# Kernel tuning notes

Measured on AMD Instinct MI355X. Metric: run time of the kernel, lower is better.

Reference implementation:

```python
import jax, jax.numpy as jnp
import numpy as np

DIM = 1024
NUM_HEADS = 16
HEAD_DIM = DIM // NUM_HEADS


def _rope_tables(seq_len, dim, dtype):
    # matches llama_rotary_embedding: inv_freq over even indices of head_dim
    inv_freq = 1.0 / (10000.0 ** (jnp.arange(0, dim, 2, dtype=jnp.float32) / dim))
    t = jnp.arange(seq_len, dtype=jnp.float32)
    freqs = jnp.outer(t, inv_freq)  # [S, dim/2]
    return jnp.cos(freqs).astype(dtype), jnp.sin(freqs).astype(dtype)


def _apply_rope(x, cos_emb, sin_emb):
    # x: [B, H, S, hd]; takes interleaved halves, concatenates rotated halves
    x1 = x[..., 0::2]
    x2 = x[..., 1::2]
    return jnp.concatenate((x1 * cos_emb - x2 * sin_emb,
                            x1 * sin_emb + x2 * cos_emb), axis=-1)


def setup_inputs() -> dict:
    key = jax.random.key(0)
    k_x, k_qkv, k_out, k_b = jax.random.split(key, 4)
    B, S, D = 2, 2048, DIM
    x = jax.random.normal(k_x, (B, S, D), dtype=jnp.float32)
    # torch nn.Linear weights are [out_features, in_features]
    w_qkv = jax.random.normal(k_qkv, (3 * D, D), dtype=jnp.float32) * (1.0 / np.sqrt(D))
    w_out = jax.random.normal(k_out, (D, D), dtype=jnp.float32) * (1.0 / np.sqrt(D))
    b_out = jax.random.normal(k_b, (D,), dtype=jnp.float32) * 0.01
    return {"x": x, "w_qkv": w_qkv, "w_out": w_out, "b_out": b_out}


def reference(x, w_qkv, w_out, b_out):
    B, S, D = x.shape
    H, hd = NUM_HEADS, HEAD_DIM
    qkv = jnp.einsum('bsd,ed->bse', x, w_qkv)  # [B, S, 3D]
    q, k, v = jnp.split(qkv, 3, axis=-1)
    # [B, S, D] -> [B, H, S, hd]
    q, k, v = (t.reshape(B, S, H, hd).transpose(0, 2, 1, 3) for t in (q, k, v))
    cos_emb, sin_emb = _rope_tables(S, hd, x.dtype)  # [S, hd/2]
    q = _apply_rope(q, cos_emb, sin_emb)
    k = _apply_rope(k, cos_emb, sin_emb)
    scores = jnp.einsum('bhqd,bhkd->bhqk', q, k) / jnp.sqrt(jnp.asarray(hd, x.dtype))
    attn = jax.nn.softmax(scores, axis=-1)
    out = jnp.einsum('bhqk,bhkd->bhqd', attn, v)
    out = out.transpose(0, 2, 1, 3).reshape(B, S, D)
    return jnp.einsum('bsd,ed->bse', out, w_out) + b_out
```

## Files before the change

### kernel.cpp

```cpp
#include <hip/hip_runtime.h>
#include <math.h>

typedef __bf16 bf16_t;
typedef bf16_t bf16x8 __attribute__((ext_vector_type(8)));
typedef bf16_t bf16x4 __attribute__((ext_vector_type(4)));
typedef short  s16x4  __attribute__((ext_vector_type(4)));
typedef float  f32x4  __attribute__((ext_vector_type(4)));

#define DIM_   1024
#define NHEADS 16
#define HDIM   64
#define SEQ    2048
#define BATCH  2

#define QK_SCALE 0.18033688011112042f

__device__ __forceinline__ s16x4 as_s16x4(bf16x4 v) {
    union { bf16x4 b; s16x4 s; } u; u.b = v; return u.s;
}

__device__ __forceinline__ void gld16(const bf16_t* g, bf16_t* l) {
    __builtin_amdgcn_global_load_lds(
        (const __attribute__((address_space(1))) void*)g,
        (__attribute__((address_space(3))) void*)l, 16, 0, 0);
}

#define XCNT   (4096u * 1024u)
#define WQCNT  (3072u * 1024u)
#define WOCNT  (1024u * 1024u)
__global__ __launch_bounds__(256) void cast3(const float* __restrict__ s0,
                                             const float* __restrict__ s1,
                                             const float* __restrict__ s2,
                                             bf16_t* __restrict__ d0,
                                             bf16_t* __restrict__ d1,
                                             bf16_t* __restrict__ d2) {
    size_t i = ((size_t)blockIdx.x * 256 + threadIdx.x) * 8;
    const float* s; bf16_t* d; size_t off;
    if (i < XCNT)               { s = s0; d = d0; off = i; }
    else if (i < XCNT + WQCNT)  { s = s1; d = d1; off = i - XCNT; }
    else                        { s = s2; d = d2; off = i - XCNT - WQCNT; }
    float4 a = *(const float4*)(s + off);
    float4 b = *(const float4*)(s + off + 4);
    bf16x8 o = { (bf16_t)a.x, (bf16_t)a.y, (bf16_t)a.z, (bf16_t)a.w,
                 (bf16_t)b.x, (bf16_t)b.y, (bf16_t)b.z, (bf16_t)b.w };
    *(bf16x8*)(d + off) = o;
}

template <bool QKV>
__global__ __launch_bounds__(256) void gemm_lds(const bf16_t* __restrict__ A,
                                                const bf16_t* __restrict__ B,
                                                const float* __restrict__ bias,
                                                void* __restrict__ Cout,
                                                bf16_t* __restrict__ vt,
                                                int M, int N, int K) {
    __shared__ __align__(16) bf16_t As[128 * 32];
    __shared__ __align__(16) bf16_t Bs[128 * 32];
    const int tid  = threadIdx.x;
    const int m0   = blockIdx.y * 128;
    const int n0   = blockIdx.x * 128;
    const int w    = tid >> 6;
    const int lane = tid & 63;
    const int m16  = lane & 15;
    const int quad = lane >> 4;
    const int wm   = (w >> 1) * 64;
    const int wn   = (w & 1) * 64;
    const int lrow = lane >> 2;
    const int lcol = (lane & 3) * 8;

    const bf16_t* pa0 = A + (size_t)(m0 + w * 16 + lrow) * K + lcol;
    const bf16_t* pb0 = B + (size_t)(n0 + w * 16 + lrow) * K + lcol;
    bf16_t* lA0 = &As[(w * 16) * 32];
    bf16_t* lA1 = &As[(64 + w * 16) * 32];
    bf16_t* lB0 = &Bs[(w * 16) * 32];
    bf16_t* lB1 = &Bs[(64 + w * 16) * 32];

    f32x4 acc[4][4] = {};

    for (int k0 = 0; k0 < K; k0 += 32) {
        __syncthreads();
        gld16(pa0 + k0, lA0);
        gld16(pa0 + (size_t)64 * K + k0, lA1);
        gld16(pb0 + k0, lB0);
        gld16(pb0 + (size_t)64 * K + k0, lB1);
        __syncthreads();

        bf16x8 af[4], bfr[4];
#pragma unroll
        for (int i = 0; i < 4; ++i)
            af[i] = *(const bf16x8*)(&As[(wm + i * 16 + m16) * 32 + quad * 8]);
#pragma unroll
        for (int j = 0; j < 4; ++j)
            bfr[j] = *(const bf16x8*)(&Bs[(wn + j * 16 + m16) * 32 + quad * 8]);
#pragma unroll
        for (int i = 0; i < 4; ++i)
#pragma unroll
            for (int j = 0; j < 4; ++j)
                acc[i][j] = __builtin_amdgcn_mfma_f32_16x16x32_bf16(af[i], bfr[j], acc[i][j], 0, 0, 0);
    }

    if (QKV && n0 >= 2 * DIM_) {
        const int b      = m0 >> 11;
        const int s_base = (m0 & (SEQ - 1)) + wm;
#pragma unroll
        for (int j = 0; j < 4; ++j) {
            const int cit = wn + j * 16 + m16;
            const int h   = ((n0 - 2 * DIM_) >> 6) + (cit >> 6);
            const int d   = cit & 63;
            bf16_t* vrow = vt + ((size_t)(b * 16 + h) * 64 + d) * SEQ + s_base;
#pragma unroll
            for (int i = 0; i < 4; ++i) {
                bf16x4 ov = { (bf16_t)acc[i][j][0], (bf16_t)acc[i][j][1],
                              (bf16_t)acc[i][j][2], (bf16_t)acc[i][j][3] };
                *(bf16x4*)(vrow + i * 16 + quad * 4) = ov;
            }
        }
    } else if (QKV) {
        bf16_t* C = (bf16_t*)Cout;
#pragma unroll
        for (int i = 0; i < 4; ++i)
#pragma unroll
            for (int j = 0; j < 4; ++j) {
                const int col = n0 + wn + j * 16 + m16;
#pragma unroll
                for (int r = 0; r < 4; ++r)
                    C[(size_t)(m0 + wm + i * 16 + quad * 4 + r) * N + col] = (bf16_t)acc[i][j][r];
            }
    } else {
        float* C = (float*)Cout;
#pragma unroll
        for (int j = 0; j < 4; ++j) {
            const int col = n0 + wn + j * 16 + m16;
            const float bv = bias[col];
#pragma unroll
            for (int i = 0; i < 4; ++i)
#pragma unroll
                for (int r = 0; r < 4; ++r)
                    C[(size_t)(m0 + wm + i * 16 + quad * 4 + r) * N + col] = acc[i][j][r] + bv;
        }
    }
}

__global__ __launch_bounds__(256) void rope_bf16(bf16_t* __restrict__ qkv) {
    __shared__ float ctab[8][32];
    __shared__ float stab[8][32];
    const int tid = threadIdx.x;
    const int sl  = tid >> 5, j = tid & 31;
    const int s   = (int)((blockIdx.x * 8 + sl) & (SEQ - 1));
    const float freq = exp2f(-0.41524101186092029f * (float)j);
    float sn, cs;
    sincosf((float)s * freq, &sn, &cs);
    ctab[sl][j] = cs;
    stab[sl][j] = sn;
    __syncthreads();

    const int gid   = blockIdx.x * 256 + tid;
    const int m     = gid >> 5;
    const int rr    = gid & 31;
    const int which = rr >> 4;
    const int hh    = rr & 15;
    const float osc = (which == 0) ? QK_SCALE : 1.0f;

    bf16_t* p = qkv + (size_t)m * (3 * DIM_) + which * DIM_ + hh * HDIM;
    union { bf16_t e[64]; bf16x8 v[8]; } X, O;
#pragma unroll
    for (int i = 0; i < 8; ++i) X.v[i] = *(const bf16x8*)(p + i * 8);
#pragma unroll
    for (int t = 0; t < 32; ++t) {
        const float x1 = (float)X.e[2 * t];
        const float x2 = (float)X.e[2 * t + 1];
        const float c  = ctab[sl][t];
        const float s2 = stab[sl][t];
        O.e[t]      = (bf16_t)((x1 * c - x2 * s2) * osc);
        O.e[32 + t] = (bf16_t)((x1 * s2 + x2 * c) * osc);
    }
#pragma unroll
    for (int i = 0; i < 8; ++i) *(bf16x8*)(p + i * 8) = O.v[i];
}

__global__ __launch_bounds__(256) void attn_mfma(const bf16_t* __restrict__ qkv,
                                                 const bf16_t* __restrict__ vt,
                                                 bf16_t* __restrict__ out) {
    __shared__ __align__(16) bf16_t Qs[64 * 72];
    __shared__ __align__(16) bf16_t Ks[64 * 72];
    __shared__ __align__(16) bf16_t Vt[64 * 72];

    const int tid  = threadIdx.x;
    const int w    = tid >> 6;
    const int lane = tid & 63;
    const int m16  = lane & 15;
    const int quad = lane >> 4;
    const int bh   = blockIdx.y;
    const int b    = bh >> 4;
    const int hh   = bh & 15;
    const int q0   = blockIdx.x * 64;

    const size_t rs = 3 * DIM_;
    const bf16_t* qbase = qkv + (size_t)(b * SEQ) * rs + hh * HDIM;
    const bf16_t* kbase = qbase + DIM_;
    const bf16_t* vtg   = vt + (size_t)bh * 64 * SEQ;

#pragma unroll
    for (int p = 0; p < 2; ++p) {
        const int idx = tid + p * 256;
        const int row = idx >> 3, c8 = (idx & 7) * 8;
        *(bf16x8*)(&Qs[row * 72 + c8]) =
            *(const bf16x8*)(qbase + (size_t)(q0 + row) * rs + c8);
    }
    __syncthreads();
    bf16x8 qf[2];
#pragma unroll
    for (int kt = 0; kt < 2; ++kt)
        qf[kt] = *(const bf16x8*)(&Qs[(w * 16 + m16) * 72 + kt * 32 + quad * 8]);

    f32x4 o[4] = {};
    float lp = 0.0f;

    for (int k0 = 0; k0 < SEQ; k0 += 64) {
#pragma unroll
        for (int p = 0; p < 2; ++p) {
            const int idx = tid + p * 256;
            const int row = idx >> 3, c8 = (idx & 7) * 8;
            *(bf16x8*)(&Ks[row * 72 + c8]) =
                *(const bf16x8*)(kbase + (size_t)(k0 + row) * rs + c8);
            *(bf16x8*)(&Vt[row * 72 + c8]) =
                *(const bf16x8*)(vtg + (size_t)row * SEQ + k0 + c8);
        }
        __syncthreads();

        f32x4 sc[4];
#pragma unroll
        for (int ks = 0; ks < 4; ++ks) {
            f32x4 c = {};
#pragma unroll
            for (int kt = 0; kt < 2; ++kt) {
                bf16x8 ak = *(const bf16x8*)(&Ks[(ks * 16 + m16) * 72 + kt * 32 + quad * 8]);
                c = __builtin_amdgcn_mfma_f32_16x16x32_bf16(ak, qf[kt], c, 0, 0, 0);
            }
            sc[ks] = c;
        }

        s16x4 pb[4];
#pragma unroll
        for (int ks = 0; ks < 4; ++ks) {
            bf16x4 pv;
#pragma unroll
            for (int r = 0; r < 4; ++r) {
                const float p = __builtin_amdgcn_exp2f(sc[ks][r]);
                lp += p;
                pv[r] = (bf16_t)p;
            }
            pb[ks] = as_s16x4(pv);
        }

#pragma unroll
        for (int ks = 0; ks < 4; ++ks) {
#pragma unroll
            for (int ds = 0; ds < 4; ++ds) {
                bf16x4 va = *(const bf16x4*)(&Vt[(ds * 16 + m16) * 72 + ks * 16 + quad * 4]);
                o[ds] = __builtin_amdgcn_mfma_f32_16x16x16bf16_1k(as_s16x4(va), pb[ks], o[ds], 0, 0, 0);
            }
        }
        __syncthreads();
    }

    lp += __shfl_xor(lp, 16);
    lp += __shfl_xor(lp, 32);
    const float inv = 1.0f / lp;

    const size_t token = (size_t)(b * SEQ + q0 + w * 16 + m16);
#pragma unroll
    for (int ds = 0; ds < 4; ++ds) {
        bf16x4 ov;
#pragma unroll
        for (int r = 0; r < 4; ++r) ov[r] = (bf16_t)(o[ds][r] * inv);
        *(bf16x4*)(out + token * DIM_ + hh * HDIM + ds * 16 + quad * 4) = ov;
    }
}

extern "C" void kernel_launch(void* const* d_in, const int* in_sizes, int n_in,
                              void* d_out, int out_size, void* d_ws, size_t ws_size,
                              hipStream_t stream) {
    const float* x     = (const float*)d_in[0];
    const float* w_qkv = (const float*)d_in[1];
    const float* w_out = (const float*)d_in[2];
    const float* b_out = (const float*)d_in[3];
    float* out = (float*)d_out;

    const int M = BATCH * SEQ;

    bf16_t* qkv_b  = (bf16_t*)d_ws;
    bf16_t* attn_b = qkv_b + (size_t)M * 3 * DIM_;
    bf16_t* vt_b   = attn_b + (size_t)M * DIM_;
    bf16_t* xb     = vt_b + (size_t)BATCH * NHEADS * HDIM * SEQ;
    bf16_t* wqkvb  = xb + (size_t)M * DIM_;
    bf16_t* woutb  = wqkvb + (size_t)3 * DIM_ * DIM_;

    cast3<<<(XCNT + WQCNT + WOCNT) / (256 * 8), 256, 0, stream>>>(
        x, w_qkv, w_out, xb, wqkvb, woutb);

    gemm_lds<true><<<dim3(3 * DIM_ / 128, M / 128), 256, 0, stream>>>(
        xb, wqkvb, nullptr, qkv_b, vt_b, M, 3 * DIM_, DIM_);

    rope_bf16<<<(M * 2 * NHEADS) / 256, 256, 0, stream>>>(qkv_b);

    attn_mfma<<<dim3(SEQ / 64, BATCH * NHEADS), 256, 0, stream>>>(qkv_b, vt_b, attn_b);

    gemm_lds<false><<<dim3(DIM_ / 128, M / 128), 256, 0, stream>>>(
        attn_b, woutb, b_out, out, nullptr, M, DIM_, DIM_);
}
```

Before: 231.1 us.

## Split attention key tile across waves and reduce partial outputs through LDS

```diff
diff --git a/kernel.cpp b/kernel.cpp
--- a/kernel.cpp
+++ b/kernel.cpp
@@ -180,9 +180,11 @@
 __global__ __launch_bounds__(256) void attn_mfma(const bf16_t* __restrict__ qkv,
                                                  const bf16_t* __restrict__ vt,
                                                  bf16_t* __restrict__ out) {
-    __shared__ __align__(16) bf16_t Qs[64 * 72];
-    __shared__ __align__(16) bf16_t Ks[64 * 72];
-    __shared__ __align__(16) bf16_t Vt[64 * 72];
+    __shared__ __align__(16) char smem[18432];
+    bf16_t* Ks   = (bf16_t*)smem;
+    bf16_t* Vt   = (bf16_t*)(smem + 9216);
+    float*  Ored = (float*)smem;
+    float*  Lred = (float*)(smem + 16640);
 
     const int tid  = threadIdx.x;
     const int w    = tid >> 6;
@@ -199,81 +201,98 @@
     const bf16_t* kbase = qbase + DIM_;
     const bf16_t* vtg   = vt + (size_t)bh * 64 * SEQ;
 
-#pragma unroll
-    for (int p = 0; p < 2; ++p) {
-        const int idx = tid + p * 256;
-        const int row = idx >> 3, c8 = (idx & 7) * 8;
-        *(bf16x8*)(&Qs[row * 72 + c8]) =
-            *(const bf16x8*)(qbase + (size_t)(q0 + row) * rs + c8);
-    }
-    __syncthreads();
-    bf16x8 qf[2];
-#pragma unroll
-    for (int kt = 0; kt < 2; ++kt)
-        qf[kt] = *(const bf16x8*)(&Qs[(w * 16 + m16) * 72 + kt * 32 + quad * 8]);
-
-    f32x4 o[4] = {};
-    float lp = 0.0f;
+    bf16x8 qf[4][2];
+#pragma unroll
+    for (int n = 0; n < 4; ++n)
+#pragma unroll
+        for (int kt = 0; kt < 2; ++kt)
+            qf[n][kt] = *(const bf16x8*)(qbase + (size_t)(q0 + n * 16 + m16) * rs + kt * 32 + quad * 8);
+
+    f32x4 o[4][4] = {};
+    float lp[4] = {};
+
+    const int srow = tid >> 3;
+    const int sc8  = (tid & 7) * 8;
 
     for (int k0 = 0; k0 < SEQ; k0 += 64) {
 #pragma unroll
         for (int p = 0; p < 2; ++p) {
-            const int idx = tid + p * 256;
-            const int row = idx >> 3, c8 = (idx & 7) * 8;
-            *(bf16x8*)(&Ks[row * 72 + c8]) =
-                *(const bf16x8*)(kbase + (size_t)(k0 + row) * rs + c8);
-            *(bf16x8*)(&Vt[row * 72 + c8]) =
-                *(const bf16x8*)(vtg + (size_t)row * SEQ + k0 + c8);
-        }
-        __syncthreads();
-
-        f32x4 sc[4];
-#pragma unroll
-        for (int ks = 0; ks < 4; ++ks) {
+            const int row = srow + p * 32;
+            *(bf16x8*)(&Ks[row * 72 + sc8]) =
+                *(const bf16x8*)(kbase + (size_t)(k0 + row) * rs + sc8);
+            *(bf16x8*)(&Vt[row * 72 + sc8]) =
+                *(const bf16x8*)(vtg + (size_t)row * SEQ + k0 + sc8);
+        }
+        __syncthreads();
+
+        bf16x8 ak[2];
+#pragma unroll
+        for (int kt = 0; kt < 2; ++kt)
+            ak[kt] = *(const bf16x8*)(&Ks[(w * 16 + m16) * 72 + kt * 32 + quad * 8]);
+
+        bf16x4 va[4];
+#pragma unroll
+        for (int ds = 0; ds < 4; ++ds)
+            va[ds] = *(const bf16x4*)(&Vt[(ds * 16 + m16) * 72 + w * 16 + quad * 4]);
+
+        s16x4 pb[4];
+#pragma unroll
+        for (int n = 0; n < 4; ++n) {
             f32x4 c = {};
 #pragma unroll
-            for (int kt = 0; kt < 2; ++kt) {
-                bf16x8 ak = *(const bf16x8*)(&Ks[(ks * 16 + m16) * 72 + kt * 32 + quad * 8]);
-                c = __builtin_amdgcn_mfma_f32_16x16x32_bf16(ak, qf[kt], c, 0, 0, 0);
-            }
-            sc[ks] = c;
-        }
-
-        s16x4 pb[4];
-#pragma unroll
-        for (int ks = 0; ks < 4; ++ks) {
+            for (int kt = 0; kt < 2; ++kt)
+                c = __builtin_amdgcn_mfma_f32_16x16x32_bf16(ak[kt], qf[n][kt], c, 0, 0, 0);
             bf16x4 pv;
 #pragma unroll
             for (int r = 0; r < 4; ++r) {
-                const float p = __builtin_amdgcn_exp2f(sc[ks][r]);
-                lp += p;
+                const float p = __builtin_amdgcn_exp2f(c[r]);
+                lp[n] += p;
                 pv[r] = (bf16_t)p;
             }
-            pb[ks] = as_s16x4(pv);
-        }
-
-#pragma unroll
-        for (int ks = 0; ks < 4; ++ks) {
-#pragma unroll
-            for (int ds = 0; ds < 4; ++ds) {
-                bf16x4 va = *(const bf16x4*)(&Vt[(ds * 16 + m16) * 72 + ks * 16 + quad * 4]);
-                o[ds] = __builtin_amdgcn_mfma_f32_16x16x16bf16_1k(as_s16x4(va), pb[ks], o[ds], 0, 0, 0);
+            pb[n] = as_s16x4(pv);
+        }
+
+#pragma unroll
+        for (int ds = 0; ds < 4; ++ds)
+#pragma unroll
+            for (int n = 0; n < 4; ++n)
+                o[ds][n] = __builtin_amdgcn_mfma_f32_16x16x16bf16_1k(as_s16x4(va[ds]), pb[n], o[ds][n], 0, 0, 0);
+        __syncthreads();
+    }
+
+#pragma unroll
+    for (int n = 0; n < 4; ++n) {
+        lp[n] += __shfl_xor(lp[n], 16);
+        lp[n] += __shfl_xor(lp[n], 32);
+    }
+    if (quad == 0) {
+#pragma unroll
+        for (int n = 0; n < 4; ++n) Lred[w * 64 + n * 16 + m16] = lp[n];
+    }
+    __syncthreads();
+    const float linv = 1.0f / (Lred[lane] + Lred[64 + lane] + Lred[128 + lane] + Lred[192 + lane]);
+
+    const size_t obase = (size_t)(b * SEQ + q0 + lane) * DIM_ + hh * HDIM;
+#pragma unroll
+    for (int p = 0; p < 4; ++p) {
+        __syncthreads();
+#pragma unroll
+        for (int n = 0; n < 4; ++n)
+#pragma unroll
+            for (int r = 0; r < 4; ++r)
+                Ored[w * 1040 + (quad * 4 + r) * 65 + n * 16 + m16] = o[p][n][r];
+        __syncthreads();
+        if (w == p) {
+            union { bf16_t e[16]; bf16x8 v[2]; } ob;
+#pragma unroll
+            for (int d = 0; d < 16; ++d) {
+                const float v = Ored[d * 65 + lane] + Ored[1040 + d * 65 + lane] +
+                                Ored[2080 + d * 65 + lane] + Ored[3120 + d * 65 + lane];
+                ob.e[d] = (bf16_t)(v * linv);
             }
-        }
-        __syncthreads();
-    }
-
-    lp += __shfl_xor(lp, 16);
-    lp += __shfl_xor(lp, 32);
-    const float inv = 1.0f / lp;
-
-    const size_t token = (size_t)(b * SEQ + q0 + w * 16 + m16);
-#pragma unroll
-    for (int ds = 0; ds < 4; ++ds) {
-        bf16x4 ov;
-#pragma unroll
-        for (int r = 0; r < 4; ++r) ov[r] = (bf16_t)(o[ds][r] * inv);
-        *(bf16x4*)(out + token * DIM_ + hh * HDIM + ds * 16 + quad * 4) = ov;
+            *(bf16x8*)(out + obase + p * 16)     = ob.v[0];
+            *(bf16x8*)(out + obase + p * 16 + 8) = ob.v[1];
+        }
     }
 }
 
```

Measured after the change: 230.5 us. Within noise of the previous version (-0.3%).
